# Kernel tuning notes

Hardware: AMD Instinct MI355X
Metric: run time of the kernel (lower is better)

The kernel has to match this reference:

```python
import jax, jax.numpy as jnp
import numpy as np

N = 131072
C = 8
W = 256


def setup_inputs() -> dict:
    key = jax.random.key(0)
    ks = jax.random.split(key, 10)
    s1 = 1.0 / np.sqrt(3.0)
    sw = 1.0 / np.sqrt(W)
    return {
        "positions": jax.random.normal(ks[0], (N, 3), dtype=jnp.float32),
        "times": jax.random.randint(ks[1], (N,), 0, C, dtype=jnp.int64),
        "W1": jax.random.normal(ks[2], (C, 3, W), dtype=jnp.float32) * s1,
        "b1": jnp.zeros((C, W), dtype=jnp.float32),
        "W2": jax.random.normal(ks[3], (C, W, W), dtype=jnp.float32) * sw,
        "b2": jnp.zeros((C, W), dtype=jnp.float32),
        "W3": jax.random.normal(ks[4], (C, W, W), dtype=jnp.float32) * sw,
        "b3": jnp.zeros((C, W), dtype=jnp.float32),
        "W4": jax.random.normal(ks[5], (C, W, 3), dtype=jnp.float32) * sw,
        "b4": jnp.zeros((C, 3), dtype=jnp.float32),
    }


def _mlp(x, w1, c1, w2, c2, w3, c3, w4, c4):
    # 4-layer MLP, Tanh hidden activations and Tanh output activation
    h = jnp.tanh(x @ w1 + c1)
    h = jnp.tanh(h @ w2 + c2)
    h = jnp.tanh(h @ w3 + c3)
    return jnp.tanh(h @ w4 + c4)


def reference(positions, times, W1, b1, W2, b2, W3, b3, W4, b4):
    # offsets = zeros_like(positions); offsets[times==i] = mlp_i(positions[times==i])
    # classes partition the points, so this equals a per-class select-sum.
    offsets = jnp.zeros_like(positions)
    for i in range(C):  # small fixed class count
        out_i = _mlp(positions, W1[i], b1[i], W2[i], b2[i], W3[i], b3[i], W4[i], b4[i])
        mask = (times == i)[:, None]  # [N,1]
        offsets = jnp.where(mask, out_i, offsets)
    return offsets
```

## Files before the change

kernel.cpp:

```cpp
#include <hip/hip_runtime.h>
#include <stdint.h>

#define N_PTS 131072
#define NCLS 8
#define MT 64
#define CAP 32768
#define PS 2.8853900817779268f

typedef __bf16 bf16x8 __attribute__((ext_vector_type(8)));
typedef float f32x4 __attribute__((ext_vector_type(4)));

__device__ __forceinline__ float exp2_fast(float a) {
#if __has_builtin(__builtin_amdgcn_exp2f)
  return __builtin_amdgcn_exp2f(a);
#else
  return exp2f(a);
#endif
}

__device__ __forceinline__ float tanh_p2(float a) {
  return fmaf(-2.0f, __builtin_amdgcn_rcpf(exp2_fast(a) + 1.0f), 1.0f);
}

__device__ __forceinline__ unsigned short f2bf_rne(float f) {
  unsigned u = __float_as_uint(f);
  u = u + 0x7fffu + ((u >> 16) & 1u);
  return (unsigned short)(u >> 16);
}

__device__ __forceinline__ unsigned pack_bf16(float a, float b) {
  unsigned ua = __float_as_uint(a) + 0x8000u;
  unsigned ub = __float_as_uint(b) + 0x8000u;
  return __builtin_amdgcn_perm(ub, ua, 0x07060302u);
}

#define PK2_BLKS 512
#define MISC_BLKS 177
#define MISC_N 45184
#define SCAT_BLKS 512
#define PREP_GRID (PK2_BLKS + MISC_BLKS + SCAT_BLKS)

__global__ __launch_bounds__(256) void k_prep(
    const int* __restrict__ times,
    const float* __restrict__ W1, const float* __restrict__ b1,
    const float* __restrict__ W2, const float* __restrict__ b2,
    const float* __restrict__ W3, const float* __restrict__ b3,
    const float* __restrict__ W4, const float* __restrict__ b4,
    int* __restrict__ hdr, int* __restrict__ sortedIdx,
    unsigned short* __restrict__ packed23,
    float* __restrict__ w1p, float* __restrict__ b2p,
    float* __restrict__ b3p, float* __restrict__ b4p,
    unsigned short* __restrict__ W4p) {
  __shared__ int lh[NCLS], lbase[NCLS];

  int b = blockIdx.x;
  int tid = threadIdx.x;

  if (b < PK2_BLKS) {
    int cl = b >> 5;
    int k8 = b & 31;
    int j = tid;
    int l = cl >> 3, c = cl & 7;
    const float* W = (l ? W3 : W2) + c * 65536 + k8 * 8 * 256 + j;
    float v0 = W[0],        v1 = W[256],     v2 = W[2 * 256], v3 = W[3 * 256];
    float v4 = W[4 * 256],  v5 = W[5 * 256], v6 = W[6 * 256], v7 = W[7 * 256];
    uint4 pk;
    pk.x = (unsigned)f2bf_rne(PS * v0) | ((unsigned)f2bf_rne(PS * v1) << 16);
    pk.y = (unsigned)f2bf_rne(PS * v2) | ((unsigned)f2bf_rne(PS * v3) << 16);
    pk.z = (unsigned)f2bf_rne(PS * v4) | ((unsigned)f2bf_rne(PS * v5) << 16);
    pk.w = (unsigned)f2bf_rne(PS * v6) | ((unsigned)f2bf_rne(PS * v7) << 16);
    *(uint4*)&packed23[cl * 65536 + (k8 * 256 + j) * 8] = pk;
  } else if (b < PK2_BLKS + MISC_BLKS) {
    int e2 = (b - PK2_BLKS) * 256 + tid;
    if (e2 < 8192) {
      int c = e2 >> 10, rem = e2 & 1023;
      int j = rem >> 2, t = rem & 3;
      float v = (t < 3) ? W1[c * 768 + t * 256 + j] : b1[c * 256 + j];
      w1p[e2] = PS * v;
    } else if (e2 < 10240) {
      int i = e2 - 8192;
      b2p[i] = PS * b2[i];
    } else if (e2 < 12288) {
      int i = e2 - 10240;
      b3p[i] = PS * b3[i];
    } else if (e2 < 12416) {
      int i = e2 - 12288;
      int c = i >> 4, r = i & 15;
      b4p[i] = (r < 3) ? PS * b4[c * 3 + r] : 0.0f;
    } else if (e2 < MISC_N) {
      int i = e2 - 12416;
      int c = i >> 12, rem = i & 4095;
      int jj = rem & 7, j = (rem >> 3) & 15, k = ((rem >> 7) << 3) + jj;
      float v = (j < 3) ? PS * W4[c * 768 + k * 3 + j] : 0.0f;
      W4p[c * 4096 + rem] = f2bf_rne(v);
    }
  } else {
    int sb = b - (PK2_BLKS + MISC_BLKS);
    if (tid < NCLS) lh[tid] = 0;
    __syncthreads();
    int i = sb * 256 + tid;
    int t = times[i];
    int r = atomicAdd(&lh[t], 1);
    __syncthreads();
    if (tid < NCLS) lbase[tid] = lh[tid] ? atomicAdd(&hdr[tid], lh[tid]) : 0;
    __syncthreads();
    sortedIdx[t * CAP + lbase[t] + r] = i;
  }
}

__global__ __launch_bounds__(256, 4) void k_mlp(
    const float* __restrict__ pos,
    const int* __restrict__ hdr, const int* __restrict__ sortedIdx,
    const unsigned short* __restrict__ packed23,
    const float* __restrict__ w1p, const float* __restrict__ b2p,
    const float* __restrict__ b3p, const float* __restrict__ b4p,
    const unsigned short* __restrict__ W4p,
    float* __restrict__ out) {

  __shared__ __align__(16) unsigned short Abuf[32][MT][8];
  __shared__ __align__(16) float4 w1i[256];
  __shared__ __align__(16) float xpos[MT][4];
  __shared__ int sIdx[MT];

  int b = blockIdx.x;
  int tid = threadIdx.x;

  int c = -1, t0 = 0, cnt = 0;
  {
    int ts = 0;
#pragma unroll
    for (int cc = 0; cc < NCLS; cc++) {
      int cc_cnt = hdr[cc];
      int tiles = (cc_cnt + MT - 1) >> 6;
      if (b >= ts && b < ts + tiles) { c = cc; t0 = b - ts; cnt = cc_cnt; }
      ts += tiles;
    }
  }
  if (c < 0) return;
  int base = c * CAP + t0 * MT;
  int mCount = min(MT, cnt - t0 * MT);

  int lane = tid & 63, w = tid >> 6;
  int quad = lane >> 4, l16 = lane & 15;
  int jbase = w * 64;

  if (tid < MT) sIdx[tid] = sortedIdx[base + min(tid, mCount - 1)];
  if (tid < MT * 3) {
    int m = tid / 3, comp = tid - 3 * m;
    int idx = sortedIdx[base + min(m, mCount - 1)];
    xpos[m][comp] = pos[idx * 3 + comp];
  }
  w1i[tid] = ((const float4*)(w1p + (size_t)c * 1024))[tid];

  const bf16x8* Af2 = (const bf16x8*)(packed23 + ((size_t)c << 16));
  const bf16x8* Af3 = (const bf16x8*)(packed23 + ((size_t)(8 + c) << 16));
  const float* bias2 = b2p + c * 256;
  const float* bias3 = b3p + c * 256;

  auto l1half = [&](int mh) {
    int m = (tid & 31) + mh * 32;
    int jq = tid >> 5;
    float x0 = xpos[m][0], x1 = xpos[m][1], x2 = xpos[m][2];
#pragma unroll
    for (int i8 = 0; i8 < 4; i8++) {
      int j8 = jq * 4 + i8;
      unsigned pk[4];
#pragma unroll
      for (int jp = 0; jp < 4; jp++) {
        float t[2];
#pragma unroll
        for (int u = 0; u < 2; u++) {
          float4 wv = w1i[j8 * 8 + jp * 2 + u];
          float a = fmaf(x0, wv.x, fmaf(x1, wv.y, fmaf(x2, wv.z, wv.w)));
          t[u] = tanh_p2(a);
        }
        pk[jp] = pack_bf16(t[0], t[1]);
      }
      *(uint4*)&Abuf[j8][m][0] = make_uint4(pk[0], pk[1], pk[2], pk[3]);
    }
  };

  auto pfun = [&](const bf16x8* __restrict__ Af, const float* __restrict__ biasp,
                  int mh, f32x4 (&acc)[4][2]) {
#pragma unroll
    for (int jf = 0; jf < 4; jf++) {
      f32x4 bv = *(const f32x4*)&biasp[jbase + jf * 16 + quad * 4];
      acc[jf][0] = bv;
      acc[jf][1] = bv;
    }
#pragma unroll
    for (int kb = 0; kb < 8; kb++) {
      int kq = kb * 4 + quad;
      bf16x8 af[4], bfr[2];
#pragma unroll
      for (int jf = 0; jf < 4; jf++)
        af[jf] = Af[kq * 256 + jbase + jf * 16 + l16];
#pragma unroll
      for (int mt = 0; mt < 2; mt++)
        bfr[mt] = *(const bf16x8*)&Abuf[kq][(mh * 2 + mt) * 16 + l16][0];
#pragma unroll
      for (int jf = 0; jf < 4; jf++)
#pragma unroll
        for (int mt = 0; mt < 2; mt++)
          acc[jf][mt] = __builtin_amdgcn_mfma_f32_16x16x32_bf16(af[jf], bfr[mt], acc[jf][mt], 0, 0, 0);
    }
  };

  auto efun = [&](f32x4 (&acc)[4][2], int mh) {
#pragma unroll
    for (int jf = 0; jf < 4; jf++) {
      int jbq = jbase + jf * 16 + quad * 4;
#pragma unroll
      for (int mt = 0; mt < 2; mt++) {
        int m = (mh * 2 + mt) * 16 + l16;
        float t0 = tanh_p2(acc[jf][mt][0]);
        float t1 = tanh_p2(acc[jf][mt][1]);
        float t2 = tanh_p2(acc[jf][mt][2]);
        float t3 = tanh_p2(acc[jf][mt][3]);
        uint2 pk = make_uint2(pack_bf16(t0, t1), pack_bf16(t2, t3));
        *(uint2*)&Abuf[jbq >> 3][m][jbq & 7] = pk;
      }
    }
  };

  f32x4 accA[4][2], accB[4][2];

  __syncthreads();
  l1half(0);
  __syncthreads();
  l1half(1);
  pfun(Af2, bias2, 0, accA);
  __syncthreads();
  pfun(Af2, bias2, 1, accB);
  efun(accA, 0);
  __syncthreads();
  efun(accB, 1);
  pfun(Af3, bias3, 0, accA);
  __syncthreads();
  pfun(Af3, bias3, 1, accB);
  efun(accA, 0);
  __syncthreads();
  efun(accB, 1);
  __syncthreads();

  {
    f32x4 acc = *(const f32x4*)&b4p[c * 16 + quad * 4];
#pragma unroll
    for (int kb = 0; kb < 8; kb++) {
      int kq = kb * 4 + quad;
      bf16x8 a4 = *(const bf16x8*)&W4p[((size_t)c * 512 + kq * 16 + l16) * 8];
      bf16x8 b4f = *(const bf16x8*)&Abuf[kq][w * 16 + l16][0];
      acc = __builtin_amdgcn_mfma_f32_16x16x32_bf16(a4, b4f, acc, 0, 0, 0);
    }
    int m = w * 16 + l16;
    if (quad == 0 && m < mCount) {
      int o = sIdx[m] * 3;
      out[o + 0] = tanh_p2(acc[0]);
      out[o + 1] = tanh_p2(acc[1]);
      out[o + 2] = tanh_p2(acc[2]);
    }
  }
}

extern "C" void kernel_launch(void* const* d_in, const int* in_sizes, int n_in,
                              void* d_out, int out_size, void* d_ws, size_t ws_size,
                              hipStream_t stream) {
  const float* pos = (const float*)d_in[0];
  const int* times = (const int*)d_in[1];
  const float* W1 = (const float*)d_in[2];
  const float* b1 = (const float*)d_in[3];
  const float* W2 = (const float*)d_in[4];
  const float* b2 = (const float*)d_in[5];
  const float* W3 = (const float*)d_in[6];
  const float* b3 = (const float*)d_in[7];
  const float* W4 = (const float*)d_in[8];
  const float* b4 = (const float*)d_in[9];

  char* ws = (char*)d_ws;
  int* hdr = (int*)ws;
  int* sortedIdx = (int*)(ws + 4096);
  float* w1p = (float*)(ws + 1052672);
  float* b2p = (float*)(ws + 1085440);
  float* b3p = (float*)(ws + 1093632);
  float* b4p = (float*)(ws + 1101824);
  unsigned short* W4p = (unsigned short*)(ws + 1102336);
  unsigned short* packed23 = (unsigned short*)(ws + (2u << 20));
  float* out = (float*)d_out;

  hipMemsetAsync(d_ws, 0, 64, stream);
  k_prep<<<PREP_GRID, 256, 0, stream>>>(times, W1, b1, W2, b2, W3, b3, W4, b4,
                                        hdr, sortedIdx, packed23,
                                        w1p, b2p, b3p, b4p, W4p);
  k_mlp<<<N_PTS / MT + NCLS, 256, 0, stream>>>(
      pos, hdr, sortedIdx, packed23, w1p, b2p, b3p, b4p, W4p, out);
}
```

Baseline: 145.4 us.

## Process two 64-point tiles per 512-thread block with ping-pong layer pipelining

The MLP kernel now uses 512 threads per block and handles 128 points as two 64-point sub-tiles, each with its own activation buffer. Each of the 8 waves computes a 32-column slice across all 64 rows of a sub-tile, so every weight fragment loaded from global memory feeds 4 MFMAs instead of 2. The MFMA k-loop of one sub-tile is interleaved with the layer-1 compute or tanh epilogue of the other. The cost is doubled LDS per block, fewer blocks in the grid, and layer 4 running on only half the waves.

```diff
diff --git a/kernel.cpp b/kernel.cpp
--- a/kernel.cpp
+++ b/kernel.cpp
@@ -3,7 +3,6 @@
 
 #define N_PTS 131072
 #define NCLS 8
-#define MT 64
 #define CAP 32768
 #define PS 2.8853900817779268f
 
@@ -108,7 +107,7 @@
   }
 }
 
-__global__ __launch_bounds__(256, 4) void k_mlp(
+__global__ __launch_bounds__(512, 4) void k_mlp(
     const float* __restrict__ pos,
     const int* __restrict__ hdr, const int* __restrict__ sortedIdx,
     const unsigned short* __restrict__ packed23,
@@ -117,10 +116,10 @@
     const unsigned short* __restrict__ W4p,
     float* __restrict__ out) {
 
-  __shared__ __align__(16) unsigned short Abuf[32][MT][8];
+  __shared__ __align__(16) unsigned short Abuf[2][32][64][8];
   __shared__ __align__(16) float4 w1i[256];
-  __shared__ __align__(16) float xpos[MT][4];
-  __shared__ int sIdx[MT];
+  __shared__ __align__(16) float xpos[2][64][4];
+  __shared__ int sIdx[2][64];
 
   int b = blockIdx.x;
   int tid = threadIdx.x;
@@ -131,135 +130,149 @@
 #pragma unroll
     for (int cc = 0; cc < NCLS; cc++) {
       int cc_cnt = hdr[cc];
-      int tiles = (cc_cnt + MT - 1) >> 6;
+      int tiles = (cc_cnt + 127) >> 7;
       if (b >= ts && b < ts + tiles) { c = cc; t0 = b - ts; cnt = cc_cnt; }
       ts += tiles;
     }
   }
   if (c < 0) return;
-  int base = c * CAP + t0 * MT;
-  int mCount = min(MT, cnt - t0 * MT);
+  int base0 = c * CAP + t0 * 128;
+  int mc0 = min(64, cnt - t0 * 128);
+  int mc1 = cnt - t0 * 128 - 64;
+  int base1 = (mc1 > 0) ? base0 + 64 : base0;
+  int mc1c = max(mc1, 1);
+  mc1 = min(mc1, 64);
 
   int lane = tid & 63, w = tid >> 6;
   int quad = lane >> 4, l16 = lane & 15;
-  int jbase = w * 64;
-
-  if (tid < MT) sIdx[tid] = sortedIdx[base + min(tid, mCount - 1)];
-  if (tid < MT * 3) {
-    int m = tid / 3, comp = tid - 3 * m;
-    int idx = sortedIdx[base + min(m, mCount - 1)];
-    xpos[m][comp] = pos[idx * 3 + comp];
-  }
-  w1i[tid] = ((const float4*)(w1p + (size_t)c * 1024))[tid];
+  int jbase = w * 32;
 
   const bf16x8* Af2 = (const bf16x8*)(packed23 + ((size_t)c << 16));
   const bf16x8* Af3 = (const bf16x8*)(packed23 + ((size_t)(8 + c) << 16));
   const float* bias2 = b2p + c * 256;
   const float* bias3 = b3p + c * 256;
 
-  auto l1half = [&](int mh) {
-    int m = (tid & 31) + mh * 32;
-    int jq = tid >> 5;
-    float x0 = xpos[m][0], x1 = xpos[m][1], x2 = xpos[m][2];
+  if (tid < 128) {
+    int t = tid >> 6, i = tid & 63;
+    int bs = t ? base1 : base0;
+    int mcc = t ? mc1c : mc0;
+    sIdx[t][i] = sortedIdx[bs + min(i, mcc - 1)];
+  }
+  if (tid < 256) w1i[tid] = ((const float4*)(w1p + (size_t)c * 1024))[tid];
+  if (tid >= 128) {
+    int e = tid - 128;
+    int m = e / 3, comp = e - 3 * m;
+    int t = m >> 6, mm = m & 63;
+    int bs = t ? base1 : base0;
+    int mcc = t ? mc1c : mc0;
+    int idx = sortedIdx[bs + min(mm, mcc - 1)];
+    xpos[t][mm][comp] = pos[idx * 3 + comp];
+  }
+
+  auto l1 = [&](int t) {
+    int m = tid & 63, jq = tid >> 6;
+    float x0 = xpos[t][m][0], x1 = xpos[t][m][1], x2 = xpos[t][m][2];
 #pragma unroll
     for (int i8 = 0; i8 < 4; i8++) {
       int j8 = jq * 4 + i8;
       unsigned pk[4];
 #pragma unroll
       for (int jp = 0; jp < 4; jp++) {
-        float t[2];
+        float tt[2];
 #pragma unroll
         for (int u = 0; u < 2; u++) {
           float4 wv = w1i[j8 * 8 + jp * 2 + u];
           float a = fmaf(x0, wv.x, fmaf(x1, wv.y, fmaf(x2, wv.z, wv.w)));
-          t[u] = tanh_p2(a);
+          tt[u] = tanh_p2(a);
         }
-        pk[jp] = pack_bf16(t[0], t[1]);
+        pk[jp] = pack_bf16(tt[0], tt[1]);
       }
-      *(uint4*)&Abuf[j8][m][0] = make_uint4(pk[0], pk[1], pk[2], pk[3]);
+      *(uint4*)&Abuf[t][j8][m][0] = make_uint4(pk[0], pk[1], pk[2], pk[3]);
     }
   };
 
-  auto pfun = [&](const bf16x8* __restrict__ Af, const float* __restrict__ biasp,
-                  int mh, f32x4 (&acc)[4][2]) {
-#pragma unroll
-    for (int jf = 0; jf < 4; jf++) {
+  auto kloop = [&](int t, const bf16x8* __restrict__ Af,
+                   const float* __restrict__ biasp, f32x4 (&acc)[2][4]) {
+#pragma unroll
+    for (int jf = 0; jf < 2; jf++) {
       f32x4 bv = *(const f32x4*)&biasp[jbase + jf * 16 + quad * 4];
-      acc[jf][0] = bv;
-      acc[jf][1] = bv;
+#pragma unroll
+      for (int mt = 0; mt < 4; mt++) acc[jf][mt] = bv;
     }
 #pragma unroll
     for (int kb = 0; kb < 8; kb++) {
       int kq = kb * 4 + quad;
-      bf16x8 af[4], bfr[2];
-#pragma unroll
-      for (int jf = 0; jf < 4; jf++)
+      bf16x8 af[2], bfr[4];
+#pragma unroll
+      for (int jf = 0; jf < 2; jf++)
         af[jf] = Af[kq * 256 + jbase + jf * 16 + l16];
 #pragma unroll
-      for (int mt = 0; mt < 2; mt++)
-        bfr[mt] = *(const bf16x8*)&Abuf[kq][(mh * 2 + mt) * 16 + l16][0];
-#pragma unroll
-      for (int jf = 0; jf < 4; jf++)
-#pragma unroll
-        for (int mt = 0; mt < 2; mt++)
+      for (int mt = 0; mt < 4; mt++)
+        bfr[mt] = *(const bf16x8*)&Abuf[t][kq][mt * 16 + l16][0];
+#pragma unroll
+      for (int jf = 0; jf < 2; jf++)
+#pragma unroll
+        for (int mt = 0; mt < 4; mt++)
           acc[jf][mt] = __builtin_amdgcn_mfma_f32_16x16x32_bf16(af[jf], bfr[mt], acc[jf][mt], 0, 0, 0);
     }
   };
 
-  auto efun = [&](f32x4 (&acc)[4][2], int mh) {
-#pragma unroll
-    for (int jf = 0; jf < 4; jf++) {
+  auto epi = [&](int t, f32x4 (&acc)[2][4]) {
+#pragma unroll
+    for (int jf = 0; jf < 2; jf++) {
       int jbq = jbase + jf * 16 + quad * 4;
 #pragma unroll
-      for (int mt = 0; mt < 2; mt++) {
-        int m = (mh * 2 + mt) * 16 + l16;
-        float t0 = tanh_p2(acc[jf][mt][0]);
-        float t1 = tanh_p2(acc[jf][mt][1]);
-        float t2 = tanh_p2(acc[jf][mt][2]);
-        float t3 = tanh_p2(acc[jf][mt][3]);
-        uint2 pk = make_uint2(pack_bf16(t0, t1), pack_bf16(t2, t3));
-        *(uint2*)&Abuf[jbq >> 3][m][jbq & 7] = pk;
+      for (int mt = 0; mt < 4; mt++) {
+        int m = mt * 16 + l16;
+        float t0_ = tanh_p2(acc[jf][mt][0]);
+        float t1_ = tanh_p2(acc[jf][mt][1]);
+        float t2_ = tanh_p2(acc[jf][mt][2]);
+        float t3_ = tanh_p2(acc[jf][mt][3]);
+        uint2 pk = make_uint2(pack_bf16(t0_, t1_), pack_bf16(t2_, t3_));
+        *(uint2*)&Abuf[t][jbq >> 3][m][jbq & 7] = pk;
       }
     }
   };
 
-  f32x4 accA[4][2], accB[4][2];
-
-  __syncthreads();
-  l1half(0);
-  __syncthreads();
-  l1half(1);
-  pfun(Af2, bias2, 0, accA);
-  __syncthreads();
-  pfun(Af2, bias2, 1, accB);
-  efun(accA, 0);
-  __syncthreads();
-  efun(accB, 1);
-  pfun(Af3, bias3, 0, accA);
-  __syncthreads();
-  pfun(Af3, bias3, 1, accB);
-  efun(accA, 0);
-  __syncthreads();
-  efun(accB, 1);
-  __syncthreads();
-
-  {
+  auto l4 = [&](int t, int mCount) {
     f32x4 acc = *(const f32x4*)&b4p[c * 16 + quad * 4];
 #pragma unroll
     for (int kb = 0; kb < 8; kb++) {
       int kq = kb * 4 + quad;
       bf16x8 a4 = *(const bf16x8*)&W4p[((size_t)c * 512 + kq * 16 + l16) * 8];
-      bf16x8 b4f = *(const bf16x8*)&Abuf[kq][w * 16 + l16][0];
+      bf16x8 b4f = *(const bf16x8*)&Abuf[t][kq][w * 16 + l16][0];
       acc = __builtin_amdgcn_mfma_f32_16x16x32_bf16(a4, b4f, acc, 0, 0, 0);
     }
     int m = w * 16 + l16;
     if (quad == 0 && m < mCount) {
-      int o = sIdx[m] * 3;
+      int o = sIdx[t][m] * 3;
       out[o + 0] = tanh_p2(acc[0]);
       out[o + 1] = tanh_p2(acc[1]);
       out[o + 2] = tanh_p2(acc[2]);
     }
-  }
+  };
+
+  f32x4 acc0[2][4], acc1[2][4];
+
+  __syncthreads();
+  l1(0);
+  __syncthreads();
+  kloop(0, Af2, bias2, acc0);
+  l1(1);
+  __syncthreads();
+  kloop(1, Af2, bias2, acc1);
+  epi(0, acc0);
+  __syncthreads();
+  kloop(0, Af3, bias3, acc0);
+  epi(1, acc1);
+  __syncthreads();
+  kloop(1, Af3, bias3, acc1);
+  epi(0, acc0);
+  __syncthreads();
+  epi(1, acc1);
+  if (w < 4) l4(0, mc0);
+  __syncthreads();
+  if (w < 4) l4(1, mc1);
 }
 
 extern "C" void kernel_launch(void* const* d_in, const int* in_sizes, int n_in,
@@ -291,6 +304,6 @@
   k_prep<<<PREP_GRID, 256, 0, stream>>>(times, W1, b1, W2, b2, W3, b3, W4, b4,
                                         hdr, sortedIdx, packed23,
                                         w1p, b2p, b3p, b4p, W4p);
-  k_mlp<<<N_PTS / MT + NCLS, 256, 0, stream>>>(
+  k_mlp<<<N_PTS / 128 + NCLS, 512, 0, stream>>>(
       pos, hdr, sortedIdx, packed23, w1p, b2p, b3p, b4p, W4p, out);
 }
```

Measured after the change: 135.6 us. 6.8% less time.
